# Performance work log

Hardware: AMD Instinct MI355X
Metric: run time of the kernel (lower is better)

The kernel has to match this reference:

```python
import jax, jax.numpy as jnp
import numpy as np

B = 131072
NF, E = 9, 8
D0 = NF * E  # 72
H = 64       # expert hidden
O = 8        # expert output
T, SE, SH = 3, 3, 3
VOCAB = 160000

PARAM_SHAPES = {
    "emb_table": (VOCAB, E),
    "spec0_W1": (T, SE, D0, H), "spec0_b1": (T, SE, H),
    "spec0_W2": (T, SE, H, O),  "spec0_b2": (T, SE, O),
    "shar0_W1": (SH, D0, H),    "shar0_b1": (SH, H),
    "shar0_W2": (SH, H, O),     "shar0_b2": (SH, O),
    "gate0_W1": (T, D0, H),     "gate0_b1": (T, H),
    "gate0_W2": (T, H, O),      "gate0_b2": (T, O),
    "gate0_W3": (T, O, SE + SH),
    "sgate0_W1": (D0, H), "sgate0_b1": (H,),
    "sgate0_W2": (H, O),  "sgate0_b2": (O,),
    "sgate0_W3": (O, T * SE + SH),
    "spec1_W1": (T, SE, O, H), "spec1_b1": (T, SE, H),
    "spec1_W2": (T, SE, H, O), "spec1_b2": (T, SE, O),
    "shar1_W1": (SH, O, H),    "shar1_b1": (SH, H),
    "shar1_W2": (SH, H, O),    "shar1_b2": (SH, O),
    "gate1_W1": (T, O, H),     "gate1_b1": (T, H),
    "gate1_W2": (T, H, O),     "gate1_b2": (T, O),
    "gate1_W3": (T, O, SE + SH),
    "tower_W": (T, O, 1), "tower_b": (T, 1),
}


def setup_inputs() -> dict:
    key = jax.random.key(0)
    keys = jax.random.split(key, len(PARAM_SHAPES) + 1)
    inp = {n: jax.random.normal(k, s, jnp.float32) * 0.1
           for (n, s), k in zip(PARAM_SHAPES.items(), keys[:-1])}
    inp["cat_idx"] = jax.random.randint(keys[-1], (B, NF), 0, VOCAB, jnp.int32)
    return inp


def _cgc(task_x, shared_x, sW1, sb1, sW2, sb2, hW1, hb1, hW2, hb2,
         gW1, gb1, gW2, gb2, gW3, sgate=None):
    """One CGC level. task_x: [T,B,in], shared_x: [B,in]."""
    # task-specific experts, batched over (task, expert)
    h = jax.nn.relu(jnp.einsum('tbi,teih->tebh', task_x, sW1) + sb1[:, :, None, :])
    spec = jax.nn.relu(jnp.einsum('tebh,teho->tebo', h, sW2) + sb2[:, :, None, :])  # [T,SE,B,O]
    # shared experts, batched over expert
    hs = jax.nn.relu(jnp.einsum('bi,eih->ebh', shared_x, hW1) + hb1[:, None, :])
    shar = jax.nn.relu(jnp.einsum('ebh,eho->ebo', hs, hW2) + hb2[:, None, :])       # [SH,B,O]
    # per-task gates: MLP[64,8] relu -> linear(no bias) -> softmax over SE+SH experts
    g = jax.nn.relu(jnp.einsum('tbi,tih->tbh', task_x, gW1) + gb1[:, None, :])
    g = jax.nn.relu(jnp.einsum('tbh,tho->tbo', g, gW2) + gb2[:, None, :])
    gw = jax.nn.softmax(jnp.einsum('tbo,toe->tbe', g, gW3), axis=-1)                # [T,B,SE+SH]
    experts = jnp.concatenate(
        [spec, jnp.broadcast_to(shar[None], (spec.shape[0],) + shar.shape)], axis=1)  # [T,SE+SH,B,O]
    task_out = jnp.einsum('tebo,tbe->tbo', experts, gw)                             # [T,B,O]
    if sgate is None:
        return task_out, None
    sgW1, sgb1, sgW2, sgb2, sgW3 = sgate
    gs = jax.nn.relu(shared_x @ sgW1 + sgb1)
    gs = jax.nn.relu(gs @ sgW2 + sgb2)
    gws = jax.nn.softmax(gs @ sgW3, axis=-1)                                        # [B,T*SE+SH]
    all_e = jnp.concatenate([spec.reshape(T * SE, spec.shape[2], O), shar], axis=0)  # [T*SE+SH,B,O]
    shared_out = jnp.einsum('ebo,be->bo', all_e, gws)
    return task_out, shared_out


def _forward(cat_idx, p):
    x = p["emb_table"][cat_idx].reshape(cat_idx.shape[0], -1)  # [B, 72]
    task_x = jnp.broadcast_to(x[None], (T,) + x.shape)
    task_x, shared_x = _cgc(
        task_x, x,
        p["spec0_W1"], p["spec0_b1"], p["spec0_W2"], p["spec0_b2"],
        p["shar0_W1"], p["shar0_b1"], p["shar0_W2"], p["shar0_b2"],
        p["gate0_W1"], p["gate0_b1"], p["gate0_W2"], p["gate0_b2"], p["gate0_W3"],
        sgate=(p["sgate0_W1"], p["sgate0_b1"], p["sgate0_W2"], p["sgate0_b2"], p["sgate0_W3"]))
    task_x, _ = _cgc(
        task_x, shared_x,
        p["spec1_W1"], p["spec1_b1"], p["spec1_W2"], p["spec1_b2"],
        p["shar1_W1"], p["shar1_b1"], p["shar1_W2"], p["shar1_b2"],
        p["gate1_W1"], p["gate1_b1"], p["gate1_W2"], p["gate1_b2"], p["gate1_W3"],
        sgate=None)
    # 3 sigmoid towers -> stacked [T, B, 1] (== dict task_0..task_2 in original)
    out = jax.nn.sigmoid(jnp.einsum('tbo,tok->tbk', task_x, p["tower_W"]) + p["tower_b"][:, None, :])
    return out


def reference(cat_idx, emb_table, spec0_W1, spec0_b1, spec0_W2, spec0_b2,
              shar0_W1, shar0_b1, shar0_W2, shar0_b2,
              gate0_W1, gate0_b1, gate0_W2, gate0_b2, gate0_W3,
              sgate0_W1, sgate0_b1, sgate0_W2, sgate0_b2, sgate0_W3,
              spec1_W1, spec1_b1, spec1_W2, spec1_b2,
              shar1_W1, shar1_b1, shar1_W2, shar1_b2,
              gate1_W1, gate1_b1, gate1_W2, gate1_b2, gate1_W3,
              tower_W, tower_b):
    p = dict(locals())
    p.pop('cat_idx')
    return _forward(cat_idx, p)
```

## Files before the change

kernel.cpp:

```cpp
#include <hip/hip_runtime.h>
#include <hip/hip_bf16.h>


#define NT 256
#define EPB 64

typedef unsigned short u16;
typedef unsigned int u32;
typedef __attribute__((ext_vector_type(8))) short short8;
typedef __attribute__((ext_vector_type(4))) float floatx4;

__device__ __forceinline__ float bflo(u32 w){ return __uint_as_float(w << 16); }
__device__ __forceinline__ float bfhi(u32 w){ return __uint_as_float(w & 0xffff0000u); }
__device__ __forceinline__ u32 f2bf(float f){
  u32 v = __float_as_uint(f);
  return (v + 0x7fffu + ((v>>16)&1u)) >> 16;
}
__device__ __forceinline__ u32 pk2(float a, float b){
  __hip_bfloat162 h2 = __float22bfloat162_rn(make_float2(a, b));
  u32 r; __builtin_memcpy(&r, &h2, sizeof(r)); return r;
}

__device__ __forceinline__ int pi2(int s){
  return (s & 3)*16 + (s >> 2);
}

#define W1F0 0
#define W2F0 49152
#define W1F1 57344
#define W2F1 72704
#define OFF_b1P0 80384
#define OFF_b2P0 81408
#define OFF_b1P1 81664
#define OFF_b2P1 82624
#define OFF_G0W3 82864
#define OFF_SG0W3 83008
#define OFF_G1W3 83104
#define OFF_TW   83248
#define OFF_Tb   83272
#define CVT_TOTAL 83275

struct PSrc { const float* p[33]; };

__global__ void cvt_kernel(PSrc S, u32* __restrict__ wsU, float* __restrict__ wsF){
  int i = blockIdx.x*256 + threadIdx.x;
  if (i >= CVT_TOTAL) return;
  if (i < 49152){
    int j2 = i & 3, l = (i>>2)&63, tt = (i>>8)&3;
    int rest = i >> 10; int s = rest % 3, u = rest / 3;
    int k0 = s*32 + (l>>4)*8 + 2*j2;
    int h  = tt*16 + (l&15);
    const float* src = (u<9)  ? S.p[0]  + (u*72)*64
                     : (u<12) ? S.p[4]  + ((u-9)*72)*64
                     : (u<15) ? S.p[8]  + ((u-12)*72)*64
                              : S.p[13];
    float lo = (k0   < 72) ? src[(k0  )*64 + h] : 0.f;
    float hi = (k0+1 < 72) ? src[(k0+1)*64 + h] : 0.f;
    wsU[i] = pk2(lo, hi);
    return;
  }
  i -= 49152;
  if (i < 8192){
    int j2 = i & 3, l = (i>>2)&63, ks = (i>>8)&1, u = i>>9;
    int s0 = ks*32 + (l>>4)*8 + 2*j2;
    int n = l & 15;
    const float* src = (u<9)  ? S.p[2]  + u*512
                     : (u<12) ? S.p[6]  + (u-9)*512
                     : (u<15) ? S.p[10] + (u-12)*512
                              : S.p[15];
    float lo = (n<8) ? src[pi2((s0  )&63)*8 + n] : 0.f;
    float hi = (n<8) ? src[pi2((s0+1)&63)*8 + n] : 0.f;
    wsU[W2F0 + i] = pk2(lo, hi);
    return;
  }
  i -= 8192;
  if (i < 15360){
    int j2 = i & 3, l = (i>>2)&63, tt = (i>>8)&3, u = i>>10;
    int k0 = (l>>4)*8 + 2*j2;
    int n = tt*16 + (l&15);
    const float* src = (u<9) ? S.p[18] + (u*8)*64
                     : (u<12) ? S.p[22] + ((u-9)*8)*64
                              : S.p[26] + ((u-12)*8)*64;
    float lo = (k0   < 8) ? src[(k0  )*64 + n] : 0.f;
    float hi = (k0+1 < 8) ? src[(k0+1)*64 + n] : 0.f;
    wsU[W1F1 + i] = pk2(lo, hi);
    return;
  }
  i -= 15360;
  if (i < 7680){
    int j2 = i & 3, l = (i>>2)&63, ks = (i>>8)&1, u = i>>9;
    int s0 = ks*32 + (l>>4)*8 + 2*j2;
    int n = l & 15;
    const float* src = (u<9) ? S.p[20] + u*512
                     : (u<12) ? S.p[24] + (u-9)*512
                              : S.p[28] + (u-12)*512;
    float lo = (n<8) ? src[pi2((s0  )&63)*8 + n] : 0.f;
    float hi = (n<8) ? src[pi2((s0+1)&63)*8 + n] : 0.f;
    wsU[W2F1 + i] = pk2(lo, hi);
    return;
  }
  i -= 7680;
  if (i < 1024){
    int u = i>>6;
    const float* src = (u<9) ? S.p[1]+u*64 : (u<12) ? S.p[5]+(u-9)*64
                     : (u<15) ? S.p[9]+(u-12)*64 : S.p[14];
    wsF[OFF_b1P0 + i] = src[i&63];
    return;
  }
  i -= 1024;
  if (i < 256){
    int u = i>>4, n = i&15;
    const float* src = (u<9) ? S.p[3]+u*8 : (u<12) ? S.p[7]+(u-9)*8
                     : (u<15) ? S.p[11]+(u-12)*8 : S.p[16];
    wsF[OFF_b2P0 + i] = (n<8) ? src[n] : 0.f;
    return;
  }
  i -= 256;
  if (i < 960){
    int u = i>>6;
    const float* src = (u<9) ? S.p[19]+u*64 : (u<12) ? S.p[23]+(u-9)*64
                               : S.p[27]+(u-12)*64;
    wsF[OFF_b1P1 + i] = src[i&63];
    return;
  }
  i -= 960;
  if (i < 240){
    int u = i>>4, n = i&15;
    const float* src = (u<9) ? S.p[21]+u*8 : (u<12) ? S.p[25]+(u-9)*8
                               : S.p[29]+(u-12)*8;
    wsF[OFF_b2P1 + i] = (n<8) ? src[n] : 0.f;
    return;
  }
  i -= 240;
  if (i < 144){ wsF[OFF_G0W3 + i] = S.p[12][i]; return; }
  i -= 144;
  if (i < 96){ wsF[OFF_SG0W3 + i] = S.p[17][i]; return; }
  i -= 96;
  if (i < 144){ wsF[OFF_G1W3 + i] = S.p[30][i]; return; }
  i -= 144;
  if (i < 24){ wsF[OFF_TW + i] = S.p[31][i]; return; }
  i -= 24;
  wsF[OFF_Tb + i] = S.p[32][i];
}

template<int N>
__device__ __forceinline__ void softmaxT(float (&v)[N]){
  float m = v[0];
  #pragma unroll
  for (int i=1;i<N;i++) m = fmaxf(m, v[i]);
  float s = 0.f;
  #pragma unroll
  for (int i=0;i<N;i++){ v[i] = __expf(v[i]-m); s += v[i]; }
  float inv = 1.f/s;
  #pragma unroll
  for (int i=0;i<N;i++) v[i] *= inv;
}

__global__ __launch_bounds__(NT, 4) void ple_kernel(
    const float* __restrict__ emb, const int* __restrict__ cat,
    const u32* __restrict__ wsU, const float* __restrict__ P,
    float* __restrict__ out, int Btot)
{
  __shared__ u32 S_[9984];
  u32* xsA = S_;
  u32* obT = S_ + 3328;
  u32* hbW = S_ + 7680;
  const int tid = threadIdx.x;
  const int e = tid & 63;
  const int su = __builtin_amdgcn_readfirstlane(tid >> 6);
  const int lane = tid & 63;
  const int q = lane >> 4;
  const int c16 = lane & 15;

  {
    const int eg = blockIdx.x*EPB + e;
    auto ldf = [&](int f){
      int idx = cat[eg*9 + f];
      const float* ep = emb + (long)idx*8;
      float4 a = *(const float4*)ep;
      float4 b = *(const float4*)(ep+4);
      uint4 w; w.x = pk2(a.x,a.y); w.y = pk2(a.z,a.w);
      w.z = pk2(b.x,b.y); w.w = pk2(b.z,b.w);
      *(uint4*)(xsA + e*52 + f*4) = w;
    };
    ldf(su); ldf(su+4);
    if (su == 0) ldf(8);
    *(uint4*)(xsA + e*52 + 36 + su*4) = (uint4){0,0,0,0};
  }
  __syncthreads();

  u16* obp = (u16*)obT;

  {
    u32* hbU = hbW + su*576;
    #pragma unroll 1
    for (int k4 = 0; k4 < 4; k4++){
      const int u = su*4 + k4;
      short8 bf[3][4];
      #pragma unroll
      for (int s=0;s<3;s++)
        #pragma unroll
        for (int t=0;t<4;t++)
          bf[s][t] = *(const short8*)(wsU + W1F0 + (((u*3+s)*4+t)*64 + lane)*4);
      float bias[4];
      #pragma unroll
      for (int t=0;t<4;t++) bias[t] = P[OFF_b1P0 + u*64 + t*16 + c16];
      const float ob2 = P[OFF_b2P0 + u*16 + c16];
      short8 w2f[2];
      #pragma unroll
      for (int ks=0;ks<2;ks++)
        w2f[ks] = *(const short8*)(wsU + W2F0 + ((u*2+ks)*64 + lane)*4);

      #pragma unroll 1
      for (int m=0;m<4;m++){
        short8 af[3];
        #pragma unroll
        for (int s=0;s<3;s++)
          af[s] = *(const short8*)(xsA + (m*16 + c16)*52 + s*16 + q*4);
        floatx4 acc[4];
        #pragma unroll
        for (int t=0;t<4;t++) acc[t] = (floatx4){bias[t],bias[t],bias[t],bias[t]};
        #pragma unroll
        for (int s=0;s<3;s++)
          #pragma unroll
          for (int t=0;t<4;t++)
            acc[t] = __builtin_amdgcn_mfma_f32_16x16x32_bf16(af[s], bf[s][t], acc[t], 0,0,0);
        #pragma unroll
        for (int r=0;r<4;r++){
          uint2 hw;
          hw.x = pk2(fmaxf(acc[0][r],0.f), fmaxf(acc[1][r],0.f));
          hw.y = pk2(fmaxf(acc[2][r],0.f), fmaxf(acc[3][r],0.f));
          *(uint2*)(hbU + (q*4+r)*36 + 2*c16) = hw;
        }
        floatx4 oc = (floatx4){ob2, ob2, ob2, ob2};
        #pragma unroll
        for (int ks=0;ks<2;ks++){
          short8 haf = *(const short8*)(hbU + c16*36 + ks*16 + q*4);
          oc = __builtin_amdgcn_mfma_f32_16x16x32_bf16(haf, w2f[ks], oc, 0,0,0);
        }
        if (c16 < 8){
          #pragma unroll
          for (int r=0;r<4;r++)
            obp[(m*16 + q*4 + r)*136 + u*8 + c16] = (u16)f2bf(fmaxf(oc[r], 0.f));
        }
      }
    }
  }
  __syncthreads();

  u32* l1in = xsA;
  *(uint4*)(l1in + e*36 + 16 + su*4) = (uint4){0,0,0,0};
  if (su < 3){
    const int t = su;
    uint4 gw = *(const uint4*)(obT + e*68 + (12+t)*4);
    float g8[8] = {bflo(gw.x),bfhi(gw.x),bflo(gw.y),bfhi(gw.y),
                   bflo(gw.z),bfhi(gw.z),bflo(gw.w),bfhi(gw.w)};
    float lg[6];
    #pragma unroll
    for (int m=0;m<6;m++){
      float s = 0.f;
      #pragma unroll
      for (int j=0;j<8;j++) s = fmaf(g8[j], P[OFF_G0W3 + t*48 + j*6 + m], s);
      lg[m] = s;
    }
    softmaxT<6>(lg);
    float in8[8] = {0,0,0,0,0,0,0,0};
    #pragma unroll
    for (int x=0;x<6;x++){
      const int uu = (x<3) ? t*3+x : 9+(x-3);
      float wv = lg[x];
      uint4 ow = *(const uint4*)(obT + e*68 + uu*4);
      in8[0] = fmaf(wv, bflo(ow.x), in8[0]); in8[1] = fmaf(wv, bfhi(ow.x), in8[1]);
      in8[2] = fmaf(wv, bflo(ow.y), in8[2]); in8[3] = fmaf(wv, bfhi(ow.y), in8[3]);
      in8[4] = fmaf(wv, bflo(ow.z), in8[4]); in8[5] = fmaf(wv, bfhi(ow.z), in8[5]);
      in8[6] = fmaf(wv, bflo(ow.w), in8[6]); in8[7] = fmaf(wv, bfhi(ow.w), in8[7]);
    }
    uint4 lw4; lw4.x = pk2(in8[0],in8[1]); lw4.y = pk2(in8[2],in8[3]);
    lw4.z = pk2(in8[4],in8[5]); lw4.w = pk2(in8[6],in8[7]);
    *(uint4*)(l1in + e*36 + t*4) = lw4;
  } else {
    uint4 gw = *(const uint4*)(obT + e*68 + 15*4);
    float g8[8] = {bflo(gw.x),bfhi(gw.x),bflo(gw.y),bfhi(gw.y),
                   bflo(gw.z),bfhi(gw.z),bflo(gw.w),bfhi(gw.w)};
    float lw[12];
    #pragma unroll
    for (int m=0;m<12;m++){
      float s = 0.f;
      #pragma unroll
      for (int j=0;j<8;j++) s = fmaf(g8[j], P[OFF_SG0W3 + j*12 + m], s);
      lw[m] = s;
    }
    softmaxT<12>(lw);
    float in8[8] = {0,0,0,0,0,0,0,0};
    #pragma unroll
    for (int uu=0;uu<12;uu++){
      float wv = lw[uu];
      uint4 ow = *(const uint4*)(obT + e*68 + uu*4);
      in8[0] = fmaf(wv, bflo(ow.x), in8[0]); in8[1] = fmaf(wv, bfhi(ow.x), in8[1]);
      in8[2] = fmaf(wv, bflo(ow.y), in8[2]); in8[3] = fmaf(wv, bfhi(ow.y), in8[3]);
      in8[4] = fmaf(wv, bflo(ow.z), in8[4]); in8[5] = fmaf(wv, bfhi(ow.z), in8[5]);
      in8[6] = fmaf(wv, bflo(ow.w), in8[6]); in8[7] = fmaf(wv, bfhi(ow.w), in8[7]);
    }
    uint4 lw4; lw4.x = pk2(in8[0],in8[1]); lw4.y = pk2(in8[2],in8[3]);
    lw4.z = pk2(in8[4],in8[5]); lw4.w = pk2(in8[6],in8[7]);
    *(uint4*)(l1in + e*36 + 12) = lw4;
  }
  __syncthreads();

  {
    u32* hbU = hbW + su*576;
    #pragma unroll 1
    for (int k4=0;k4<4;k4++){
      const int u = su*4 + k4;
      if (u >= 15) break;
      const int base_u = (u<9) ? (u/3)*4 : ((u<12) ? 12 : (u-12)*4);
      const int aoff = (q==0) ? base_u : (16 + q*4);
      short8 bf1[4];
      #pragma unroll
      for (int t=0;t<4;t++)
        bf1[t] = *(const short8*)(wsU + W1F1 + ((u*4+t)*64 + lane)*4);
      float bias[4];
      #pragma unroll
      for (int t=0;t<4;t++) bias[t] = P[OFF_b1P1 + u*64 + t*16 + c16];
      const float ob2 = P[OFF_b2P1 + u*16 + c16];
      short8 w2f[2];
      #pragma unroll
      for (int ks=0;ks<2;ks++)
        w2f[ks] = *(const short8*)(wsU + W2F1 + ((u*2+ks)*64 + lane)*4);

      #pragma unroll 1
      for (int m=0;m<4;m++){
        short8 af = *(const short8*)(l1in + (m*16 + c16)*36 + aoff);
        floatx4 acc[4];
        #pragma unroll
        for (int t=0;t<4;t++) acc[t] = (floatx4){bias[t],bias[t],bias[t],bias[t]};
        #pragma unroll
        for (int t=0;t<4;t++)
          acc[t] = __builtin_amdgcn_mfma_f32_16x16x32_bf16(af, bf1[t], acc[t], 0,0,0);
        #pragma unroll
        for (int r=0;r<4;r++){
          uint2 hw;
          hw.x = pk2(fmaxf(acc[0][r],0.f), fmaxf(acc[1][r],0.f));
          hw.y = pk2(fmaxf(acc[2][r],0.f), fmaxf(acc[3][r],0.f));
          *(uint2*)(hbU + (q*4+r)*36 + 2*c16) = hw;
        }
        floatx4 oc = (floatx4){ob2, ob2, ob2, ob2};
        #pragma unroll
        for (int ks=0;ks<2;ks++){
          short8 haf = *(const short8*)(hbU + c16*36 + ks*16 + q*4);
          oc = __builtin_amdgcn_mfma_f32_16x16x32_bf16(haf, w2f[ks], oc, 0,0,0);
        }
        if (c16 < 8){
          #pragma unroll
          for (int r=0;r<4;r++)
            obp[(m*16 + q*4 + r)*136 + u*8 + c16] = (u16)f2bf(fmaxf(oc[r], 0.f));
        }
      }
    }
  }
  __syncthreads();

  if (su < 3){
    const int t = su;
    uint4 gw = *(const uint4*)(obT + e*68 + (12+t)*4);
    float g8[8] = {bflo(gw.x),bfhi(gw.x),bflo(gw.y),bfhi(gw.y),
                   bflo(gw.z),bfhi(gw.z),bflo(gw.w),bfhi(gw.w)};
    float lg[6];
    #pragma unroll
    for (int m=0;m<6;m++){
      float s = 0.f;
      #pragma unroll
      for (int j=0;j<8;j++) s = fmaf(g8[j], P[OFF_G1W3 + t*48 + j*6 + m], s);
      lg[m] = s;
    }
    softmaxT<6>(lg);
    float t1[8] = {0,0,0,0,0,0,0,0};
    #pragma unroll
    for (int x=0;x<6;x++){
      const int uu = (x<3) ? t*3+x : 9+(x-3);
      float wv = lg[x];
      uint4 ow = *(const uint4*)(obT + e*68 + uu*4);
      t1[0] = fmaf(wv, bflo(ow.x), t1[0]); t1[1] = fmaf(wv, bfhi(ow.x), t1[1]);
      t1[2] = fmaf(wv, bflo(ow.y), t1[2]); t1[3] = fmaf(wv, bfhi(ow.y), t1[3]);
      t1[4] = fmaf(wv, bflo(ow.z), t1[4]); t1[5] = fmaf(wv, bfhi(ow.z), t1[5]);
      t1[6] = fmaf(wv, bflo(ow.w), t1[6]); t1[7] = fmaf(wv, bfhi(ow.w), t1[7]);
    }
    float s = P[OFF_Tb + t];
    #pragma unroll
    for (int j=0;j<8;j++) s = fmaf(t1[j], P[OFF_TW + t*8 + j], s);
    out[t*Btot + blockIdx.x*EPB + e] = 1.f/(1.f + __expf(-s));
  }
}

extern "C" void kernel_launch(void* const* d_in, const int* in_sizes, int n_in,
                              void* d_out, int out_size, void* d_ws, size_t ws_size,
                              hipStream_t stream)
{
  const float* emb = (const float*)d_in[0];
  const int* cat = (const int*)d_in[34];
  float* out = (float*)d_out;
  u32* wsU = (u32*)d_ws;
  float* wsF = (float*)d_ws;
  PSrc S;
  for (int k=0;k<33;k++) S.p[k] = (const float*)d_in[k+1];
  const int B = in_sizes[34] / 9;

  cvt_kernel<<<(CVT_TOTAL+255)/256, 256, 0, stream>>>(S, wsU, wsF);
  ple_kernel<<<B/EPB, NT, 0, stream>>>(emb, cat, wsU, wsF, out, B);
}
```

Measured before the change: 194.9 us.

## Switch bf16 path to fp16 MFMA with transposed expert-output layout and dot2 gating

Converts weights and activations from bf16 to fp16, using the packed round-toward-zero conversion and f16 MFMA. The expert-output scratch is transposed to be output-dim-major so the gate-weighted combine can use packed fp16 dot2 instructions over 12 experts at once. Bias loads become a single float4 after permuting biases in the conversion kernel. The aim is cheaper conversions and fewer scalar FMAs in the combine, at the cost of fp16 range limits and round-toward-zero precision.

```diff
diff --git a/kernel.cpp b/kernel.cpp
--- a/kernel.cpp
+++ b/kernel.cpp
@@ -1,5 +1,4 @@
 #include <hip/hip_runtime.h>
-#include <hip/hip_bf16.h>
 
 
 #define NT 256
@@ -7,18 +6,23 @@
 
 typedef unsigned short u16;
 typedef unsigned int u32;
-typedef __attribute__((ext_vector_type(8))) short short8;
+typedef __fp16 hv2 __attribute__((ext_vector_type(2)));
+typedef __fp16 half8 __attribute__((ext_vector_type(8)));
 typedef __attribute__((ext_vector_type(4))) float floatx4;
 
-__device__ __forceinline__ float bflo(u32 w){ return __uint_as_float(w << 16); }
-__device__ __forceinline__ float bfhi(u32 w){ return __uint_as_float(w & 0xffff0000u); }
-__device__ __forceinline__ u32 f2bf(float f){
-  u32 v = __float_as_uint(f);
-  return (v + 0x7fffu + ((v>>16)&1u)) >> 16;
-}
-__device__ __forceinline__ u32 pk2(float a, float b){
-  __hip_bfloat162 h2 = __float22bfloat162_rn(make_float2(a, b));
-  u32 r; __builtin_memcpy(&r, &h2, sizeof(r)); return r;
+__device__ __forceinline__ u32 pkh2(float a, float b){
+  hv2 v = __builtin_amdgcn_cvt_pkrtz(a, b);
+  u32 r; __builtin_memcpy(&r, &v, 4); return r;
+}
+__device__ __forceinline__ u16 f2h(float a){
+  __fp16 h = (__fp16)a; u16 r; __builtin_memcpy(&r, &h, 2); return r;
+}
+__device__ __forceinline__ float h2f(u16 v){
+  __fp16 h; __builtin_memcpy(&h, &v, 2); return (float)h;
+}
+__device__ __forceinline__ float dot2(u32 a, u32 b, float c){
+  hv2 av, bv; __builtin_memcpy(&av, &a, 4); __builtin_memcpy(&bv, &b, 4);
+  return __builtin_amdgcn_fdot2(av, bv, c, false);
 }
 
 __device__ __forceinline__ int pi2(int s){
@@ -56,7 +60,7 @@
                               : S.p[13];
     float lo = (k0   < 72) ? src[(k0  )*64 + h] : 0.f;
     float hi = (k0+1 < 72) ? src[(k0+1)*64 + h] : 0.f;
-    wsU[i] = pk2(lo, hi);
+    wsU[i] = pkh2(lo, hi);
     return;
   }
   i -= 49152;
@@ -70,7 +74,7 @@
                               : S.p[15];
     float lo = (n<8) ? src[pi2((s0  )&63)*8 + n] : 0.f;
     float hi = (n<8) ? src[pi2((s0+1)&63)*8 + n] : 0.f;
-    wsU[W2F0 + i] = pk2(lo, hi);
+    wsU[W2F0 + i] = pkh2(lo, hi);
     return;
   }
   i -= 8192;
@@ -83,7 +87,7 @@
                               : S.p[26] + ((u-12)*8)*64;
     float lo = (k0   < 8) ? src[(k0  )*64 + n] : 0.f;
     float hi = (k0+1 < 8) ? src[(k0+1)*64 + n] : 0.f;
-    wsU[W1F1 + i] = pk2(lo, hi);
+    wsU[W1F1 + i] = pkh2(lo, hi);
     return;
   }
   i -= 15360;
@@ -96,15 +100,15 @@
                               : S.p[28] + (u-12)*512;
     float lo = (n<8) ? src[pi2((s0  )&63)*8 + n] : 0.f;
     float hi = (n<8) ? src[pi2((s0+1)&63)*8 + n] : 0.f;
-    wsU[W2F1 + i] = pk2(lo, hi);
+    wsU[W2F1 + i] = pkh2(lo, hi);
     return;
   }
   i -= 7680;
   if (i < 1024){
-    int u = i>>6;
+    int u = i>>6, r = i&63, c16 = r>>2, t = r&3;
     const float* src = (u<9) ? S.p[1]+u*64 : (u<12) ? S.p[5]+(u-9)*64
                      : (u<15) ? S.p[9]+(u-12)*64 : S.p[14];
-    wsF[OFF_b1P0 + i] = src[i&63];
+    wsF[OFF_b1P0 + i] = src[t*16 + c16];
     return;
   }
   i -= 1024;
@@ -117,10 +121,10 @@
   }
   i -= 256;
   if (i < 960){
-    int u = i>>6;
+    int u = i>>6, r = i&63, c16 = r>>2, t = r&3;
     const float* src = (u<9) ? S.p[19]+u*64 : (u<12) ? S.p[23]+(u-9)*64
                                : S.p[27]+(u-12)*64;
-    wsF[OFF_b1P1 + i] = src[i&63];
+    wsF[OFF_b1P1 + i] = src[t*16 + c16];
     return;
   }
   i -= 960;
@@ -179,8 +183,8 @@
       const float* ep = emb + (long)idx*8;
       float4 a = *(const float4*)ep;
       float4 b = *(const float4*)(ep+4);
-      uint4 w; w.x = pk2(a.x,a.y); w.y = pk2(a.z,a.w);
-      w.z = pk2(b.x,b.y); w.w = pk2(b.z,b.w);
+      uint4 w; w.x = pkh2(a.x,a.y); w.y = pkh2(a.z,a.w);
+      w.z = pkh2(b.x,b.y); w.w = pkh2(b.z,b.w);
       *(uint4*)(xsA + e*52 + f*4) = w;
     };
     ldf(su); ldf(su+4);
@@ -196,27 +200,26 @@
     #pragma unroll 1
     for (int k4 = 0; k4 < 4; k4++){
       const int u = su*4 + k4;
-      short8 bf[3][4];
+      half8 bf[3][4];
       #pragma unroll
       for (int s=0;s<3;s++)
         #pragma unroll
         for (int t=0;t<4;t++)
-          bf[s][t] = *(const short8*)(wsU + W1F0 + (((u*3+s)*4+t)*64 + lane)*4);
-      float bias[4];
-      #pragma unroll
-      for (int t=0;t<4;t++) bias[t] = P[OFF_b1P0 + u*64 + t*16 + c16];
+          bf[s][t] = *(const half8*)(wsU + W1F0 + (((u*3+s)*4+t)*64 + lane)*4);
+      float4 bias4 = *(const float4*)(P + OFF_b1P0 + u*64 + c16*4);
+      float bias[4] = {bias4.x, bias4.y, bias4.z, bias4.w};
       const float ob2 = P[OFF_b2P0 + u*16 + c16];
-      short8 w2f[2];
+      half8 w2f[2];
       #pragma unroll
       for (int ks=0;ks<2;ks++)
-        w2f[ks] = *(const short8*)(wsU + W2F0 + ((u*2+ks)*64 + lane)*4);
+        w2f[ks] = *(const half8*)(wsU + W2F0 + ((u*2+ks)*64 + lane)*4);
 
       #pragma unroll 1
       for (int m=0;m<4;m++){
-        short8 af[3];
+        half8 af[3];
         #pragma unroll
         for (int s=0;s<3;s++)
-          af[s] = *(const short8*)(xsA + (m*16 + c16)*52 + s*16 + q*4);
+          af[s] = *(const half8*)(xsA + (m*16 + c16)*52 + s*16 + q*4);
         floatx4 acc[4];
         #pragma unroll
         for (int t=0;t<4;t++) acc[t] = (floatx4){bias[t],bias[t],bias[t],bias[t]};
@@ -224,24 +227,24 @@
         for (int s=0;s<3;s++)
           #pragma unroll
           for (int t=0;t<4;t++)
-            acc[t] = __builtin_amdgcn_mfma_f32_16x16x32_bf16(af[s], bf[s][t], acc[t], 0,0,0);
+            acc[t] = __builtin_amdgcn_mfma_f32_16x16x32_f16(af[s], bf[s][t], acc[t], 0,0,0);
         #pragma unroll
         for (int r=0;r<4;r++){
           uint2 hw;
-          hw.x = pk2(fmaxf(acc[0][r],0.f), fmaxf(acc[1][r],0.f));
-          hw.y = pk2(fmaxf(acc[2][r],0.f), fmaxf(acc[3][r],0.f));
+          hw.x = pkh2(fmaxf(acc[0][r],0.f), fmaxf(acc[1][r],0.f));
+          hw.y = pkh2(fmaxf(acc[2][r],0.f), fmaxf(acc[3][r],0.f));
           *(uint2*)(hbU + (q*4+r)*36 + 2*c16) = hw;
         }
         floatx4 oc = (floatx4){ob2, ob2, ob2, ob2};
         #pragma unroll
         for (int ks=0;ks<2;ks++){
-          short8 haf = *(const short8*)(hbU + c16*36 + ks*16 + q*4);
-          oc = __builtin_amdgcn_mfma_f32_16x16x32_bf16(haf, w2f[ks], oc, 0,0,0);
+          half8 haf = *(const half8*)(hbU + c16*36 + ks*16 + q*4);
+          oc = __builtin_amdgcn_mfma_f32_16x16x32_f16(haf, w2f[ks], oc, 0,0,0);
         }
         if (c16 < 8){
           #pragma unroll
           for (int r=0;r<4;r++)
-            obp[(m*16 + q*4 + r)*136 + u*8 + c16] = (u16)f2bf(fmaxf(oc[r], 0.f));
+            obp[(m*16 + q*4 + r)*136 + c16*16 + u] = f2h(fmaxf(oc[r], 0.f));
         }
       }
     }
@@ -250,60 +253,65 @@
 
   u32* l1in = xsA;
   *(uint4*)(l1in + e*36 + 16 + su*4) = (uint4){0,0,0,0};
-  if (su < 3){
-    const int t = su;
-    uint4 gw = *(const uint4*)(obT + e*68 + (12+t)*4);
-    float g8[8] = {bflo(gw.x),bfhi(gw.x),bflo(gw.y),bfhi(gw.y),
-                   bflo(gw.z),bfhi(gw.z),bflo(gw.w),bfhi(gw.w)};
-    float lg[6];
-    #pragma unroll
-    for (int m=0;m<6;m++){
-      float s = 0.f;
-      #pragma unroll
-      for (int j=0;j<8;j++) s = fmaf(g8[j], P[OFF_G0W3 + t*48 + j*6 + m], s);
-      lg[m] = s;
-    }
-    softmaxT<6>(lg);
-    float in8[8] = {0,0,0,0,0,0,0,0};
-    #pragma unroll
-    for (int x=0;x<6;x++){
-      const int uu = (x<3) ? t*3+x : 9+(x-3);
-      float wv = lg[x];
-      uint4 ow = *(const uint4*)(obT + e*68 + uu*4);
-      in8[0] = fmaf(wv, bflo(ow.x), in8[0]); in8[1] = fmaf(wv, bfhi(ow.x), in8[1]);
-      in8[2] = fmaf(wv, bflo(ow.y), in8[2]); in8[3] = fmaf(wv, bfhi(ow.y), in8[3]);
-      in8[4] = fmaf(wv, bflo(ow.z), in8[4]); in8[5] = fmaf(wv, bfhi(ow.z), in8[5]);
-      in8[6] = fmaf(wv, bflo(ow.w), in8[6]); in8[7] = fmaf(wv, bfhi(ow.w), in8[7]);
-    }
-    uint4 lw4; lw4.x = pk2(in8[0],in8[1]); lw4.y = pk2(in8[2],in8[3]);
-    lw4.z = pk2(in8[4],in8[5]); lw4.w = pk2(in8[6],in8[7]);
-    *(uint4*)(l1in + e*36 + t*4) = lw4;
-  } else {
-    uint4 gw = *(const uint4*)(obT + e*68 + 15*4);
-    float g8[8] = {bflo(gw.x),bfhi(gw.x),bflo(gw.y),bfhi(gw.y),
-                   bflo(gw.z),bfhi(gw.z),bflo(gw.w),bfhi(gw.w)};
-    float lw[12];
-    #pragma unroll
-    for (int m=0;m<12;m++){
-      float s = 0.f;
-      #pragma unroll
-      for (int j=0;j<8;j++) s = fmaf(g8[j], P[OFF_SG0W3 + j*12 + m], s);
-      lw[m] = s;
-    }
-    softmaxT<12>(lw);
-    float in8[8] = {0,0,0,0,0,0,0,0};
-    #pragma unroll
-    for (int uu=0;uu<12;uu++){
-      float wv = lw[uu];
-      uint4 ow = *(const uint4*)(obT + e*68 + uu*4);
-      in8[0] = fmaf(wv, bflo(ow.x), in8[0]); in8[1] = fmaf(wv, bfhi(ow.x), in8[1]);
-      in8[2] = fmaf(wv, bflo(ow.y), in8[2]); in8[3] = fmaf(wv, bfhi(ow.y), in8[3]);
-      in8[4] = fmaf(wv, bflo(ow.z), in8[4]); in8[5] = fmaf(wv, bfhi(ow.z), in8[5]);
-      in8[6] = fmaf(wv, bflo(ow.w), in8[6]); in8[7] = fmaf(wv, bfhi(ow.w), in8[7]);
-    }
-    uint4 lw4; lw4.x = pk2(in8[0],in8[1]); lw4.y = pk2(in8[2],in8[3]);
-    lw4.z = pk2(in8[4],in8[5]); lw4.w = pk2(in8[6],in8[7]);
-    *(uint4*)(l1in + e*36 + 12) = lw4;
+  {
+    float wv12[12];
+    {
+      const int ug = (su<3) ? 12+su : 15;
+      float g8[8];
+      #pragma unroll
+      for (int j=0;j<8;j++) g8[j] = h2f(obp[e*136 + j*16 + ug]);
+      if (su < 3){
+        const int t = su;
+        float lg[6];
+        #pragma unroll
+        for (int m=0;m<6;m++){
+          float s = 0.f;
+          #pragma unroll
+          for (int j=0;j<8;j++) s = fmaf(g8[j], P[OFF_G0W3 + t*48 + j*6 + m], s);
+          lg[m] = s;
+        }
+        softmaxT<6>(lg);
+        #pragma unroll
+        for (int k=0;k<12;k++) wv12[k] = 0.f;
+        #pragma unroll
+        for (int x=0;x<3;x++) wv12[t*3+x] = lg[x];
+        #pragma unroll
+        for (int s3=0;s3<3;s3++) wv12[9+s3] = lg[3+s3];
+      } else {
+        float lw[12];
+        #pragma unroll
+        for (int m=0;m<12;m++){
+          float s = 0.f;
+          #pragma unroll
+          for (int j=0;j<8;j++) s = fmaf(g8[j], P[OFF_SG0W3 + j*12 + m], s);
+          lw[m] = s;
+        }
+        softmaxT<12>(lw);
+        #pragma unroll
+        for (int k=0;k<12;k++) wv12[k] = lw[k];
+      }
+    }
+    u32 wp[6];
+    #pragma unroll
+    for (int p=0;p<6;p++) wp[p] = pkh2(wv12[2*p], wv12[2*p+1]);
+    float in8[8];
+    #pragma unroll
+    for (int n=0;n<8;n++){
+      const u32* rowp = obT + e*68 + n*8;
+      uint4 A = *(const uint4*)rowp;
+      uint2 Bv = *(const uint2*)(rowp + 4);
+      float s = dot2(A.x, wp[0], 0.f);
+      s = dot2(A.y, wp[1], s);
+      s = dot2(A.z, wp[2], s);
+      s = dot2(A.w, wp[3], s);
+      s = dot2(Bv.x, wp[4], s);
+      s = dot2(Bv.y, wp[5], s);
+      in8[n] = s;
+    }
+    const int dst = (su<3) ? su*4 : 12;
+    uint4 lw4; lw4.x = pkh2(in8[0],in8[1]); lw4.y = pkh2(in8[2],in8[3]);
+    lw4.z = pkh2(in8[4],in8[5]); lw4.w = pkh2(in8[6],in8[7]);
+    *(uint4*)(l1in + e*36 + dst) = lw4;
   }
   __syncthreads();
 
@@ -315,45 +323,44 @@
       if (u >= 15) break;
       const int base_u = (u<9) ? (u/3)*4 : ((u<12) ? 12 : (u-12)*4);
       const int aoff = (q==0) ? base_u : (16 + q*4);
-      short8 bf1[4];
+      half8 bf1[4];
       #pragma unroll
       for (int t=0;t<4;t++)
-        bf1[t] = *(const short8*)(wsU + W1F1 + ((u*4+t)*64 + lane)*4);
-      float bias[4];
-      #pragma unroll
-      for (int t=0;t<4;t++) bias[t] = P[OFF_b1P1 + u*64 + t*16 + c16];
+        bf1[t] = *(const half8*)(wsU + W1F1 + ((u*4+t)*64 + lane)*4);
+      float4 bias4 = *(const float4*)(P + OFF_b1P1 + u*64 + c16*4);
+      float bias[4] = {bias4.x, bias4.y, bias4.z, bias4.w};
       const float ob2 = P[OFF_b2P1 + u*16 + c16];
-      short8 w2f[2];
+      half8 w2f[2];
       #pragma unroll
       for (int ks=0;ks<2;ks++)
-        w2f[ks] = *(const short8*)(wsU + W2F1 + ((u*2+ks)*64 + lane)*4);
+        w2f[ks] = *(const half8*)(wsU + W2F1 + ((u*2+ks)*64 + lane)*4);
 
       #pragma unroll 1
       for (int m=0;m<4;m++){
-        short8 af = *(const short8*)(l1in + (m*16 + c16)*36 + aoff);
+        half8 af = *(const half8*)(l1in + (m*16 + c16)*36 + aoff);
         floatx4 acc[4];
         #pragma unroll
         for (int t=0;t<4;t++) acc[t] = (floatx4){bias[t],bias[t],bias[t],bias[t]};
         #pragma unroll
         for (int t=0;t<4;t++)
-          acc[t] = __builtin_amdgcn_mfma_f32_16x16x32_bf16(af, bf1[t], acc[t], 0,0,0);
+          acc[t] = __builtin_amdgcn_mfma_f32_16x16x32_f16(af, bf1[t], acc[t], 0,0,0);
         #pragma unroll
         for (int r=0;r<4;r++){
           uint2 hw;
-          hw.x = pk2(fmaxf(acc[0][r],0.f), fmaxf(acc[1][r],0.f));
-          hw.y = pk2(fmaxf(acc[2][r],0.f), fmaxf(acc[3][r],0.f));
+          hw.x = pkh2(fmaxf(acc[0][r],0.f), fmaxf(acc[1][r],0.f));
+          hw.y = pkh2(fmaxf(acc[2][r],0.f), fmaxf(acc[3][r],0.f));
           *(uint2*)(hbU + (q*4+r)*36 + 2*c16) = hw;
         }
         floatx4 oc = (floatx4){ob2, ob2, ob2, ob2};
         #pragma unroll
         for (int ks=0;ks<2;ks++){
-          short8 haf = *(const short8*)(hbU + c16*36 + ks*16 + q*4);
-          oc = __builtin_amdgcn_mfma_f32_16x16x32_bf16(haf, w2f[ks], oc, 0,0,0);
+          half8 haf = *(const half8*)(hbU + c16*36 + ks*16 + q*4);
+          oc = __builtin_amdgcn_mfma_f32_16x16x32_f16(haf, w2f[ks], oc, 0,0,0);
         }
         if (c16 < 8){
           #pragma unroll
           for (int r=0;r<4;r++)
-            obp[(m*16 + q*4 + r)*136 + u*8 + c16] = (u16)f2bf(fmaxf(oc[r], 0.f));
+            obp[(m*16 + q*4 + r)*136 + c16*16 + u] = f2h(fmaxf(oc[r], 0.f));
         }
       }
     }
@@ -362,9 +369,9 @@
 
   if (su < 3){
     const int t = su;
-    uint4 gw = *(const uint4*)(obT + e*68 + (12+t)*4);
-    float g8[8] = {bflo(gw.x),bfhi(gw.x),bflo(gw.y),bfhi(gw.y),
-                   bflo(gw.z),bfhi(gw.z),bflo(gw.w),bfhi(gw.w)};
+    float g8[8];
+    #pragma unroll
+    for (int j=0;j<8;j++) g8[j] = h2f(obp[e*136 + j*16 + 12+t]);
     float lg[6];
     #pragma unroll
     for (int m=0;m<6;m++){
@@ -374,20 +381,30 @@
       lg[m] = s;
     }
     softmaxT<6>(lg);
-    float t1[8] = {0,0,0,0,0,0,0,0};
-    #pragma unroll
-    for (int x=0;x<6;x++){
-      const int uu = (x<3) ? t*3+x : 9+(x-3);
-      float wv = lg[x];
-      uint4 ow = *(const uint4*)(obT + e*68 + uu*4);
-      t1[0] = fmaf(wv, bflo(ow.x), t1[0]); t1[1] = fmaf(wv, bfhi(ow.x), t1[1]);
-      t1[2] = fmaf(wv, bflo(ow.y), t1[2]); t1[3] = fmaf(wv, bfhi(ow.y), t1[3]);
-      t1[4] = fmaf(wv, bflo(ow.z), t1[4]); t1[5] = fmaf(wv, bfhi(ow.z), t1[5]);
-      t1[6] = fmaf(wv, bflo(ow.w), t1[6]); t1[7] = fmaf(wv, bfhi(ow.w), t1[7]);
-    }
+    float wv12[12];
+    #pragma unroll
+    for (int k=0;k<12;k++) wv12[k] = 0.f;
+    #pragma unroll
+    for (int x=0;x<3;x++) wv12[t*3+x] = lg[x];
+    #pragma unroll
+    for (int s3=0;s3<3;s3++) wv12[9+s3] = lg[3+s3];
+    u32 wp[6];
+    #pragma unroll
+    for (int p=0;p<6;p++) wp[p] = pkh2(wv12[2*p], wv12[2*p+1]);
     float s = P[OFF_Tb + t];
     #pragma unroll
-    for (int j=0;j<8;j++) s = fmaf(t1[j], P[OFF_TW + t*8 + j], s);
+    for (int n=0;n<8;n++){
+      const u32* rowp = obT + e*68 + n*8;
+      uint4 A = *(const uint4*)rowp;
+      uint2 Bv = *(const uint2*)(rowp + 4);
+      float v = dot2(A.x, wp[0], 0.f);
+      v = dot2(A.y, wp[1], v);
+      v = dot2(A.z, wp[2], v);
+      v = dot2(A.w, wp[3], v);
+      v = dot2(Bv.x, wp[4], v);
+      v = dot2(Bv.y, wp[5], v);
+      s = fmaf(v, P[OFF_TW + t*8 + n], s);
+    }
     out[t*Btot + blockIdx.x*EPB + e] = 1.f/(1.f + __expf(-s));
   }
 }
```

New measurement: 192.8 us. Within noise of the previous version (-1.1%).
